# Kernel tuning notes

Measured on AMD Instinct MI355X. Metric: run time of the kernel, lower is better.

The kernel has to match this reference:

```python
import jax, jax.numpy as jnp
import numpy as np

B, S, HID = 1, 2048, 4096
N_HEADS, N_KV_HEADS = 32, 8
HEAD_DIM = HID // N_HEADS  # 128


def setup_inputs() -> dict:
    key = jax.random.key(0)
    ks = jax.random.split(key, 5)
    w = 0.02  # init scale for weights
    return {
        "hidden_states": jax.random.normal(ks[0], (B, S, HID), dtype=jnp.float32),
        "Wq": jax.random.normal(ks[1], (HID, HID), dtype=jnp.float32) * w,
        "Wk": jax.random.normal(ks[2], (N_KV_HEADS * HEAD_DIM, HID), dtype=jnp.float32) * w,
        "Wv": jax.random.normal(ks[3], (N_KV_HEADS * HEAD_DIM, HID), dtype=jnp.float32) * w,
        "Wo": jax.random.normal(ks[4], (HID, HID), dtype=jnp.float32) * w,
        "n_init": 4,
        "n_local": 1024,
    }


def reference(hidden_states, Wq, Wk, Wv, Wo, n_init, n_local):
    b, s, hid = hidden_states.shape
    n_rep = N_HEADS // N_KV_HEADS
    scale = 1.0 / np.sqrt(HEAD_DIM).astype(np.float32)

    # QKV projections (torch Linear: y = x @ W.T)
    q = (hidden_states @ Wq.T).reshape(b, s, N_HEADS, HEAD_DIM).transpose(0, 2, 1, 3)
    k = (hidden_states @ Wk.T).reshape(b, s, N_KV_HEADS, HEAD_DIM).transpose(0, 2, 1, 3)
    v = (hidden_states @ Wv.T).reshape(b, s, N_KV_HEADS, HEAD_DIM).transpose(0, 2, 1, 3)

    # GQA: repeat KV heads to match query heads
    k = jnp.repeat(k, n_rep, axis=1)  # [b, H, s, d]
    v = jnp.repeat(v, n_rep, axis=1)

    scores = jnp.einsum('bhqd,bhkd->bhqk', q, k) * scale  # [b, H, s, s]

    # StreamingLLM mask: causal AND (attention sink OR sliding window)
    i = jnp.arange(s)[:, None]
    j = jnp.arange(s)[None, :]
    allowed = (j <= i) & ((j < n_init) | (i - j < n_local))  # [s, s]
    neg = jnp.finfo(scores.dtype).min
    scores = jnp.where(allowed[None, None], scores, neg)

    probs = jax.nn.softmax(scores, axis=-1)
    attn = jnp.einsum('bhqk,bhkd->bhqd', probs, v)  # [b, H, s, d]
    attn = attn.transpose(0, 2, 1, 3).reshape(b, s, hid)
    return attn @ Wo.T
```

## Files before the change

### kernel.cpp

```cpp
#include <hip/hip_runtime.h>
#include <hip/hip_bf16.h>

#define S     2048
#define HID   4096
#define NH    32
#define NKV   8
#define DH    128
#define KVD   1024
#define NQK   6144
#define KDIM  4096

typedef unsigned short ushort_t;
typedef __attribute__((ext_vector_type(8))) __bf16 bf16x8;
typedef __attribute__((ext_vector_type(8))) unsigned short u16x8;
typedef __attribute__((ext_vector_type(4))) float f32x4;

static __device__ __forceinline__ unsigned short f2b(float f) {
    union { float f; unsigned int i; } x; x.f = f;
    unsigned int r = (x.i + 0x7fffu + ((x.i >> 16) & 1u)) >> 16;
    return (unsigned short)r;
}

static __device__ __forceinline__ void gload16(const void* g, void* l) {
    __builtin_amdgcn_global_load_lds(
        (const __attribute__((address_space(1))) void*)g,
        (__attribute__((address_space(3))) void*)l, 16, 0, 0);
}

__global__ __launch_bounds__(256)
void cvt_f2b(const float* __restrict__ src, ushort_t* __restrict__ dst, int n4) {
    int i = blockIdx.x * 256 + threadIdx.x;
    if (i < n4) {
        float4 v = ((const float4*)src)[i];
        ushort4 o;
        o.x = f2b(v.x); o.y = f2b(v.y); o.z = f2b(v.z); o.w = f2b(v.w);
        ((ushort4*)dst)[i] = o;
    }
}

#define G_BM 256
#define G_BN 128
#define G_BK 64
#define BUF_USH ((G_BM + G_BN) * G_BK)
#define BOFF_B  (G_BM * G_BK)

#define STG_A(bb, kt2, j) gload16(gA[j] + (size_t)(kt2) * G_BK, &sm[(bb) + ldA[j]])
#define STG_B(bb, kt2, j) gload16(gB[j] + (size_t)(kt2) * G_BK, &sm[(bb) + ldB[j]])

template <int MODE>
__global__ __launch_bounds__(512, 2)
void gemm256(const ushort_t* __restrict__ A, const ushort_t* __restrict__ B,
             float* __restrict__ Cf, ushort_t* __restrict__ Qb,
             ushort_t* __restrict__ Kb, ushort_t* __restrict__ Vt,
             int M, int N, int K) {
    __shared__ __align__(16) ushort_t sm[3 * BUF_USH];

    const int tid   = threadIdx.x;
    const int w     = tid >> 6;
    const int lane  = tid & 63;
    const int mlane = lane & 15;
    const int q4    = lane >> 4;
    const int wr    = w >> 1, wc = w & 1;
    const int m0    = blockIdx.y * G_BM;
    const int n0    = blockIdx.x * G_BN;

    const ushort_t* gA[4];
    const ushort_t* gB[2];
    int ldA[4], ldB[2];
#pragma unroll
    for (int j = 0; j < 4; j++) {
        int c = j * 512 + tid, row = c >> 3, sl = (c & 7) ^ (row & 7);
        gA[j]  = A + (size_t)(m0 + row) * K + sl * 8;
        ldA[j] = (j * 512 + w * 64) * 8;
    }
#pragma unroll
    for (int j = 0; j < 2; j++) {
        int c = j * 512 + tid, row = c >> 3, sl = (c & 7) ^ (row & 7);
        gB[j]  = B + (size_t)(n0 + row) * K + sl * 8;
        ldB[j] = BOFF_B + (j * 512 + w * 64) * 8;
    }

    int offA[4][2], offB[4][2];
#pragma unroll
    for (int f = 0; f < 4; f++)
#pragma unroll
        for (int ks = 0; ks < 2; ks++) {
            int ra = wr * 64 + f * 16 + mlane;
            offA[f][ks] = ra * 64 + (((ks * 4 + q4) ^ (ra & 7)) * 8);
            int rb = wc * 64 + f * 16 + mlane;
            offB[f][ks] = BOFF_B + rb * 64 + (((ks * 4 + q4) ^ (rb & 7)) * 8);
        }

    f32x4 acc[4][4];
#pragma unroll
    for (int i = 0; i < 4; i++)
#pragma unroll
        for (int j = 0; j < 4; j++) acc[i][j] = (f32x4)(0.0f);

    const int NT = K / G_BK;

    STG_A(0, 0, 0); STG_A(0, 0, 1); STG_A(0, 0, 2); STG_A(0, 0, 3);
    STG_B(0, 0, 0); STG_B(0, 0, 1);
    STG_A(BUF_USH, 1, 0); STG_A(BUF_USH, 1, 1);
    STG_A(BUF_USH, 1, 2); STG_A(BUF_USH, 1, 3);
    STG_B(BUF_USH, 1, 0); STG_B(BUF_USH, 1, 1);
    asm volatile("s_waitcnt vmcnt(6)" ::: "memory");
    __builtin_amdgcn_s_barrier();

    bf16x8 afc[4], bqc[4], afn[4], bqn[4];
#pragma unroll
    for (int f = 0; f < 4; f++) {
        afc[f] = *(const bf16x8*)&sm[offA[f][0]];
        bqc[f] = *(const bf16x8*)&sm[offB[f][0]];
    }

    int s_cur = 0;
    for (int kt = 0; kt < NT; kt++) {
        const int s_n1 = (s_cur == 2) ? 0 : s_cur + 1;
        const int s_n2 = (s_n1  == 2) ? 0 : s_n1  + 1;
        const int base = s_cur * BUF_USH;
        const int b1   = s_n1 * BUF_USH;
        const int b2   = s_n2 * BUF_USH;
        const bool stg = (kt + 2) < NT;

#pragma unroll
        for (int f = 0; f < 4; f++) {
            afn[f] = *(const bf16x8*)&sm[base + offA[f][1]];
            bqn[f] = *(const bf16x8*)&sm[base + offB[f][1]];
        }
        if (stg) { STG_A(b2, kt + 2, 0); STG_A(b2, kt + 2, 1); STG_B(b2, kt + 2, 0); }
        __builtin_amdgcn_sched_barrier(0);
        __builtin_amdgcn_s_setprio(1);
#pragma unroll
        for (int mt = 0; mt < 4; mt++)
#pragma unroll
            for (int nt = 0; nt < 4; nt++)
                acc[mt][nt] = __builtin_amdgcn_mfma_f32_16x16x32_bf16(
                    afc[mt], bqc[nt], acc[mt][nt], 0, 0, 0);
        __builtin_amdgcn_s_setprio(0);
        if (stg) asm volatile("s_waitcnt vmcnt(3)" ::: "memory");
        else     asm volatile("s_waitcnt vmcnt(0)" ::: "memory");
        __builtin_amdgcn_s_barrier();

#pragma unroll
        for (int f = 0; f < 4; f++) {
            afc[f] = *(const bf16x8*)&sm[b1 + offA[f][0]];
            bqc[f] = *(const bf16x8*)&sm[b1 + offB[f][0]];
        }
        if (stg) { STG_A(b2, kt + 2, 2); STG_A(b2, kt + 2, 3); STG_B(b2, kt + 2, 1); }
        __builtin_amdgcn_sched_barrier(0);
        __builtin_amdgcn_s_setprio(1);
#pragma unroll
        for (int mt = 0; mt < 4; mt++)
#pragma unroll
            for (int nt = 0; nt < 4; nt++)
                acc[mt][nt] = __builtin_amdgcn_mfma_f32_16x16x32_bf16(
                    afn[mt], bqn[nt], acc[mt][nt], 0, 0, 0);
        __builtin_amdgcn_s_setprio(0);
        __builtin_amdgcn_s_barrier();
        __builtin_amdgcn_sched_barrier(0);
        s_cur = s_n1;
    }

#pragma unroll
    for (int fm = 0; fm < 4; fm++) {
#pragma unroll
        for (int fn = 0; fn < 4; fn++) {
            const int row = m0 + wr * 64 + fm * 16 + q4 * 4;
            const int col = n0 + wc * 64 + fn * 16 + mlane;
            if (MODE == 0) {
#pragma unroll
                for (int r = 0; r < 4; r++)
                    Cf[(size_t)(row + r) * N + col] = acc[fm][fn][r];
            } else {
                if (n0 < HID) {
#pragma unroll
                    for (int r = 0; r < 4; r++)
                        Qb[(size_t)(row + r) * HID + col] = f2b(acc[fm][fn][r]);
                } else if (n0 < HID + KVD) {
                    int c2 = col - HID;
#pragma unroll
                    for (int r = 0; r < 4; r++)
                        Kb[(size_t)(row + r) * KVD + c2] = f2b(acc[fm][fn][r]);
                } else {
                    int c2 = col - (HID + KVD);
                    ushort4 o;
                    o.x = f2b(acc[fm][fn][0]); o.y = f2b(acc[fm][fn][1]);
                    o.z = f2b(acc[fm][fn][2]); o.w = f2b(acc[fm][fn][3]);
                    *(ushort4*)(Vt + (size_t)c2 * S + row) = o;
                }
            }
        }
    }
}

__global__ __launch_bounds__(256)
void attn_mfma(const ushort_t* __restrict__ Qb, const ushort_t* __restrict__ Kb,
               const ushort_t* __restrict__ Vt, ushort_t* __restrict__ O,
               const int* __restrict__ n_init_p, const int* __restrict__ n_local_p) {
    __shared__ ushort_t Ks[4][32][40];
    __shared__ ushort_t Vs[128][40];
    __shared__ ushort_t Ps[4][16][40];

    const int n_init = *n_init_p, n_local = *n_local_p;
    const int tid   = threadIdx.x;
    const int w     = tid >> 6;
    const int lane  = tid & 63;
    const int mlane = lane & 15;
    const int q4    = lane >> 4;
    const int h     = blockIdx.x >> 5;
    const int qt    = blockIdx.x & 31;
    const int kh    = h >> 2;
    const int i0    = qt * 64;
    const int iMax  = i0 + 63;
    const int qrow_base = i0 + w * 16;

    bf16x8 qf[4];
    {
        const ushort_t* qp = Qb + (size_t)(qrow_base + mlane) * HID + h * DH + q4 * 8;
#pragma unroll
        for (int ks = 0; ks < 4; ks++) qf[ks] = *(const bf16x8*)(qp + ks * 32);
    }

    f32x4 oacc[8];
#pragma unroll
    for (int i = 0; i < 8; i++) oacc[i] = (f32x4)(0.0f);
    float lrow[4];
#pragma unroll
    for (int r = 0; r < 4; r++) lrow[r] = 0.0f;

    int wstart = i0 - n_local + 1; if (wstart < 0) wstart = 0;
    const int tw   = (wstart <= n_init) ? 0 : (wstart >> 5);
    const int tmax = iMax >> 5;
    const float scale = 0.08838834764831845f;

    const int skk = tid >> 4, sc = tid & 15;
    const int vd  = tid >> 2, vc = tid & 3;
    ushort_t* psw = &Ps[w][0][0];

    const ushort_t* kbase = Kb + (size_t)kh * DH;
    const ushort_t* vbase = Vt + (size_t)(kh * DH) * S;

    u16x8 ka, kc, va, vb;
    {
        const int j0 = 0;
        ka = *(const u16x8*)(kbase + (size_t)(j0 + skk) * KVD + sc * 8);
        kc = *(const u16x8*)(kbase + (size_t)(j0 + skk + 16) * KVD + sc * 8);
        va = *(const u16x8*)(vbase + (size_t)vd * S + j0 + vc * 8);
        vb = *(const u16x8*)(vbase + (size_t)(vd + 64) * S + j0 + vc * 8);
    }

    int t = 0;
    while (t <= tmax) {
        const int j0 = t * 32;
        const int tnxt = (t == 0) ? ((tw > 1) ? tw : 1) : t + 1;

        __syncthreads();
        *(u16x8*)&Ks[sc >> 2][skk][(sc & 3) * 8] = ka;
        *(u16x8*)&Ks[sc >> 2][skk + 16][(sc & 3) * 8] = kc;
        *(u16x8*)&Vs[vd][vc * 8] = va;
        *(u16x8*)&Vs[vd + 64][vc * 8] = vb;
        __syncthreads();

        if (tnxt <= tmax) {
            const int jn = tnxt * 32;
            ka = *(const u16x8*)(kbase + (size_t)(jn + skk) * KVD + sc * 8);
            kc = *(const u16x8*)(kbase + (size_t)(jn + skk + 16) * KVD + sc * 8);
            va = *(const u16x8*)(vbase + (size_t)vd * S + jn + vc * 8);
            vb = *(const u16x8*)(vbase + (size_t)(vd + 64) * S + jn + vc * 8);
        }

        f32x4 sacc0 = (f32x4)(0.0f), sacc1 = (f32x4)(0.0f);
#pragma unroll
        for (int ks = 0; ks < 4; ks++) {
            bf16x8 k0f = *(const bf16x8*)&Ks[ks][mlane][q4 * 8];
            bf16x8 k1f = *(const bf16x8*)&Ks[ks][16 + mlane][q4 * 8];
            sacc0 = __builtin_amdgcn_mfma_f32_16x16x32_bf16(qf[ks], k0f, sacc0, 0, 0, 0);
            sacc1 = __builtin_amdgcn_mfma_f32_16x16x32_bf16(qf[ks], k1f, sacc1, 0, 0, 0);
        }

        const bool interior = (j0 + 31 <= i0) && (iMax - j0 < n_local);

#pragma unroll
        for (int r = 0; r < 4; r++) {
            float p0, p1;
            if (interior) {
                p0 = __expf(sacc0[r] * scale);
                p1 = __expf(sacc1[r] * scale);
            } else {
                int qi = qrow_base + q4 * 4 + r;
                int jA = j0 + mlane, jB = jA + 16;
                bool okA = (jA <= qi) && ((jA < n_init) || (qi - jA < n_local));
                bool okB = (jB <= qi) && ((jB < n_init) || (qi - jB < n_local));
                p0 = okA ? __expf(sacc0[r] * scale) : 0.0f;
                p1 = okB ? __expf(sacc1[r] * scale) : 0.0f;
            }
            lrow[r] += p0 + p1;
            psw[(q4 * 4 + r) * 40 + mlane]      = f2b(p0);
            psw[(q4 * 4 + r) * 40 + 16 + mlane] = f2b(p1);
        }

        bf16x8 pf = *(const bf16x8*)&psw[mlane * 40 + q4 * 8];
#pragma unroll
        for (int dt = 0; dt < 8; dt++) {
            bf16x8 vf = *(const bf16x8*)&Vs[dt * 16 + mlane][q4 * 8];
            oacc[dt] = __builtin_amdgcn_mfma_f32_16x16x32_bf16(pf, vf, oacc[dt], 0, 0, 0);
        }

        t = tnxt;
    }

#pragma unroll
    for (int r = 0; r < 4; r++) {
#pragma unroll
        for (int off = 1; off < 16; off <<= 1)
            lrow[r] += __shfl_xor(lrow[r], off);
    }

#pragma unroll
    for (int r = 0; r < 4; r++) {
        float inv = 1.0f / lrow[r];
        int qrow = qrow_base + q4 * 4 + r;
        ushort_t* op = O + (size_t)qrow * HID + h * DH + mlane;
#pragma unroll
        for (int dt = 0; dt < 8; dt++)
            op[dt * 16] = f2b(oacc[dt][r] * inv);
    }
}

extern "C" void kernel_launch(void* const* d_in, const int* in_sizes, int n_in,
                              void* d_out, int out_size, void* d_ws, size_t ws_size,
                              hipStream_t stream) {
    const float* H  = (const float*)d_in[0];
    const float* Wq = (const float*)d_in[1];
    const float* Wk = (const float*)d_in[2];
    const float* Wv = (const float*)d_in[3];
    const float* Wo = (const float*)d_in[4];
    const int* n_init_p  = (const int*)d_in[5];
    const int* n_local_p = (const int*)d_in[6];

    char* p = (char*)d_ws;
    ushort_t* Hb   = (ushort_t*)p;  p += (size_t)S * HID * 2;
    ushort_t* Wbuf = (ushort_t*)p;  p += (size_t)NQK * KDIM * 2;
    ushort_t* Qb   = (ushort_t*)p;  p += (size_t)S * HID * 2;
    ushort_t* Kb   = (ushort_t*)p;  p += (size_t)S * KVD * 2;
    ushort_t* Vt   = (ushort_t*)p;
    ushort_t* Ab   = Hb;

    dim3 blk(256);
    const int nH = S * HID / 4, nWq = HID * KDIM / 4, nWk = KVD * KDIM / 4;

    cvt_f2b<<<dim3((nH  + 255) / 256), blk, 0, stream>>>(H,  Hb, nH);
    cvt_f2b<<<dim3((nWq + 255) / 256), blk, 0, stream>>>(Wq, Wbuf, nWq);
    cvt_f2b<<<dim3((nWk + 255) / 256), blk, 0, stream>>>(Wk, Wbuf + (size_t)HID * KDIM, nWk);
    cvt_f2b<<<dim3((nWk + 255) / 256), blk, 0, stream>>>(Wv, Wbuf + (size_t)(HID + KVD) * KDIM, nWk);
    gemm256<1><<<dim3(NQK / G_BN, S / G_BM), dim3(512), 0, stream>>>(
        Hb, Wbuf, nullptr, Qb, Kb, Vt, S, NQK, KDIM);
    attn_mfma<<<dim3(NH * (S / 64)), blk, 0, stream>>>(Qb, Kb, Vt, Ab, n_init_p, n_local_p);
    cvt_f2b<<<dim3((nWq + 255) / 256), blk, 0, stream>>>(Wo, Wbuf, nWq);
    gemm256<0><<<dim3(HID / G_BN, S / G_BM), dim3(512), 0, stream>>>(
        Ab, Wbuf, (float*)d_out, nullptr, nullptr, nullptr, S, HID, KDIM);
}
```

Before: 460.8 us.

## Add 256x256 tile QKV GEMM with 4-stage LDS pipeline

Adds a dedicated QKV projection GEMM that uses 256x256 output tiles with BK=32 and a 4-buffer global-to-LDS prefetch pipeline. Loads are issued three tiles ahead and gated by explicit vmcnt waits, and MFMA runs at raised priority. The larger tile is meant to raise arithmetic intensity and cut global traffic per FLOP, while the deeper pipeline hides load latency. The trade-offs are a grid of only 24x8 blocks, which may underfill the GPU, and higher register pressure from 32 accumulator fragments per thread.

```diff
diff --git a/kernel.cpp b/kernel.cpp
--- a/kernel.cpp
+++ b/kernel.cpp
@@ -35,6 +35,127 @@
         ushort4 o;
         o.x = f2b(v.x); o.y = f2b(v.y); o.z = f2b(v.z); o.w = f2b(v.w);
         ((ushort4*)dst)[i] = o;
+    }
+}
+
+#define Q_BM  256
+#define Q_BN  256
+#define Q_BK  32
+#define QBUF  ((Q_BM + Q_BN) * Q_BK)
+#define QBOFF (Q_BM * Q_BK)
+
+__global__ __launch_bounds__(512, 2)
+void gemmq(const ushort_t* __restrict__ A, const ushort_t* __restrict__ B,
+           ushort_t* __restrict__ Qb, ushort_t* __restrict__ Kb,
+           ushort_t* __restrict__ Vt, int K) {
+    __shared__ __align__(16) ushort_t sm[4 * QBUF];
+
+    const int tid   = threadIdx.x;
+    const int w     = tid >> 6;
+    const int lane  = tid & 63;
+    const int mlane = lane & 15;
+    const int q4    = lane >> 4;
+    const int wr    = w >> 2, wc = w & 3;
+    const int m0    = blockIdx.y * Q_BM;
+    const int n0    = blockIdx.x * Q_BN;
+
+    const ushort_t* gA[2];
+    const ushort_t* gB[2];
+    int ldA[2], ldB[2];
+#pragma unroll
+    for (int j = 0; j < 2; j++) {
+        int c = j * 512 + tid, row = c >> 2, sl = (c & 3) ^ ((row >> 1) & 3);
+        gA[j]  = A + (size_t)(m0 + row) * K + sl * 8;
+        ldA[j] = (j * 512 + w * 64) * 8;
+        gB[j]  = B + (size_t)(n0 + row) * K + sl * 8;
+        ldB[j] = QBOFF + (j * 512 + w * 64) * 8;
+    }
+
+    int offA[8], offB[4];
+#pragma unroll
+    for (int f = 0; f < 8; f++) {
+        int ra = wr * 128 + f * 16 + mlane;
+        offA[f] = ra * 32 + ((q4 ^ ((ra >> 1) & 3)) * 8);
+    }
+#pragma unroll
+    for (int f = 0; f < 4; f++) {
+        int rb = wc * 64 + f * 16 + mlane;
+        offB[f] = QBOFF + rb * 32 + ((q4 ^ ((rb >> 1) & 3)) * 8);
+    }
+
+    f32x4 acc[8][4];
+#pragma unroll
+    for (int i = 0; i < 8; i++)
+#pragma unroll
+        for (int j = 0; j < 4; j++) acc[i][j] = (f32x4)(0.0f);
+
+    const int NT = K / Q_BK;
+
+#pragma unroll
+    for (int t = 0; t < 3; t++) {
+#pragma unroll
+        for (int j = 0; j < 2; j++) {
+            gload16(gA[j] + (size_t)t * Q_BK, &sm[t * QBUF + ldA[j]]);
+            gload16(gB[j] + (size_t)t * Q_BK, &sm[t * QBUF + ldB[j]]);
+        }
+    }
+    asm volatile("s_waitcnt vmcnt(8)" ::: "memory");
+    __builtin_amdgcn_s_barrier();
+
+    for (int kt = 0; kt < NT; kt++) {
+        const int base = (kt & 3) * QBUF;
+        const int b3   = ((kt + 3) & 3) * QBUF;
+        const bool stg = (kt + 3) < NT;
+
+        bf16x8 af[8], bq[4];
+#pragma unroll
+        for (int f = 0; f < 8; f++) af[f] = *(const bf16x8*)&sm[base + offA[f]];
+#pragma unroll
+        for (int f = 0; f < 4; f++) bq[f] = *(const bf16x8*)&sm[base + offB[f]];
+
+        if (stg) {
+            gload16(gA[0] + (size_t)(kt + 3) * Q_BK, &sm[b3 + ldA[0]]);
+            gload16(gA[1] + (size_t)(kt + 3) * Q_BK, &sm[b3 + ldA[1]]);
+            gload16(gB[0] + (size_t)(kt + 3) * Q_BK, &sm[b3 + ldB[0]]);
+            gload16(gB[1] + (size_t)(kt + 3) * Q_BK, &sm[b3 + ldB[1]]);
+        }
+        __builtin_amdgcn_sched_barrier(0);
+        __builtin_amdgcn_s_setprio(1);
+#pragma unroll
+        for (int mt = 0; mt < 8; mt++)
+#pragma unroll
+            for (int nt = 0; nt < 4; nt++)
+                acc[mt][nt] = __builtin_amdgcn_mfma_f32_16x16x32_bf16(
+                    af[mt], bq[nt], acc[mt][nt], 0, 0, 0);
+        __builtin_amdgcn_s_setprio(0);
+        if (stg) asm volatile("s_waitcnt vmcnt(4)" ::: "memory");
+        else     asm volatile("s_waitcnt vmcnt(0)" ::: "memory");
+        __builtin_amdgcn_s_barrier();
+    }
+
+#pragma unroll
+    for (int fm = 0; fm < 8; fm++) {
+#pragma unroll
+        for (int fn = 0; fn < 4; fn++) {
+            const int row = m0 + wr * 128 + fm * 16 + q4 * 4;
+            const int col = n0 + wc * 64 + fn * 16 + mlane;
+            if (n0 < HID) {
+#pragma unroll
+                for (int r = 0; r < 4; r++)
+                    Qb[(size_t)(row + r) * HID + col] = f2b(acc[fm][fn][r]);
+            } else if (n0 < HID + KVD) {
+                int c2 = col - HID;
+#pragma unroll
+                for (int r = 0; r < 4; r++)
+                    Kb[(size_t)(row + r) * KVD + c2] = f2b(acc[fm][fn][r]);
+            } else {
+                int c2 = col - (HID + KVD);
+                ushort4 o;
+                o.x = f2b(acc[fm][fn][0]); o.y = f2b(acc[fm][fn][1]);
+                o.z = f2b(acc[fm][fn][2]); o.w = f2b(acc[fm][fn][3]);
+                *(ushort4*)(Vt + (size_t)c2 * S + row) = o;
+            }
+        }
     }
 }
 
@@ -354,8 +475,8 @@
     cvt_f2b<<<dim3((nWq + 255) / 256), blk, 0, stream>>>(Wq, Wbuf, nWq);
     cvt_f2b<<<dim3((nWk + 255) / 256), blk, 0, stream>>>(Wk, Wbuf + (size_t)HID * KDIM, nWk);
     cvt_f2b<<<dim3((nWk + 255) / 256), blk, 0, stream>>>(Wv, Wbuf + (size_t)(HID + KVD) * KDIM, nWk);
-    gemm256<1><<<dim3(NQK / G_BN, S / G_BM), dim3(512), 0, stream>>>(
-        Hb, Wbuf, nullptr, Qb, Kb, Vt, S, NQK, KDIM);
+    gemmq<<<dim3(NQK / Q_BN, S / Q_BM), dim3(512), 0, stream>>>(
+        Hb, Wbuf, Qb, Kb, Vt, KDIM);
     attn_mfma<<<dim3(NH * (S / 64)), blk, 0, stream>>>(Qb, Kb, Vt, Ab, n_init_p, n_local_p);
     cvt_f2b<<<dim3((nWq + 255) / 256), blk, 0, stream>>>(Wo, Wbuf, nWq);
     gemm256<0><<<dim3(HID / G_BN, S / G_BM), dim3(512), 0, stream>>>(
```

New measurement: 453.5 us. No clear change (-1.6%).
